# Optimization experiments

Hardware: AMD Instinct MI355X
Metric: run time of the kernel (lower is better)

## Reference

```python
import jax, jax.numpy as jnp
import numpy as np

N, D = 8192, 512
LOGIT_SCALE = 2.659


def setup_inputs() -> dict:
    key = jax.random.key(0)
    k1, k2, k3 = jax.random.split(key, 3)
    text_features = jax.random.normal(k1, (N, D), dtype=jnp.float32)
    image_features = jax.random.normal(k2, (N, D), dtype=jnp.float32)
    labels = jax.random.randint(k3, (N,), 0, 100, dtype=jnp.int64)
    # sprinkle in some -1 (unlabeled) entries like the original supports
    labels = jnp.where(jax.random.uniform(jax.random.fold_in(key, 7), (N,)) < 0.1, -1, labels)
    return {"text_features": text_features, "image_features": image_features, "labels": labels}


def _l2_normalize(x):
    n = jnp.sqrt(jnp.sum(x * x, axis=-1, keepdims=True))
    return x / jnp.maximum(n, 1e-12)


def _soft_ce(s, t):
    # -(t * log softmax(s)).sum(-1) / t.sum(-1), averaged over rows
    loss = -jnp.sum(t * jax.nn.log_softmax(s, axis=-1), axis=-1)
    return jnp.mean(loss / jnp.sum(t, axis=-1))


def reference(text_features, image_features, labels):
    img = _l2_normalize(image_features)
    txt = _l2_normalize(text_features)
    logits_per_image = LOGIT_SCALE * (img @ txt.T)   # [N, N]
    logits_per_text = LOGIT_SCALE * (txt @ img.T)    # [N, N]

    # Vectorized equivalent of the per-row loop:
    # T[i,j] = 1 if i == j else (labels[i] == labels[j] and labels[i] != -1)
    eq = (labels[:, None] == labels[None, :]) & (labels[:, None] != -1)
    n = labels.shape[0]
    target = jnp.where(jnp.eye(n, dtype=bool), 1.0, eq.astype(jnp.float32))

    return (_soft_ce(logits_per_image, target) + _soft_ce(logits_per_text, target)) / 2
```

## Files before the change

kernel.cpp:

```cpp
#include <hip/hip_runtime.h>
#include <hip/hip_bf16.h>

#define N_ROWS 8192
#define DIM 512
#define SCALE 2.659f
#define MAXLOGIT 2.659f
#define LOG2E 1.4426950408889634f
#define NCHUNK 16
#define CHUNK 512
#define BM 128
#define BN 128
#define NCLS 128

typedef __attribute__((ext_vector_type(8))) short short8;
typedef __attribute__((ext_vector_type(4))) float f32x4;

__device__ __forceinline__ unsigned short f2bf(float f) {
    unsigned int u = __float_as_uint(f);
    u += 0x7fffu + ((u >> 16) & 1u);
    return (unsigned short)(u >> 16);
}
__device__ __forceinline__ float bf2f(unsigned short s) {
    return __uint_as_float((unsigned)s << 16);
}

__global__ __launch_bounds__(256) void norm_cast_kernel(
    const float* __restrict__ text, const float* __restrict__ image,
    const int* __restrict__ labels,
    unsigned short* __restrict__ imgn, unsigned short* __restrict__ txtn,
    float4* __restrict__ zbase, float* __restrict__ sd, float* __restrict__ out)
{
    if (blockIdx.x < 16) {
        zbase[blockIdx.x * 256 + threadIdx.x] = make_float4(0.f, 0.f, 0.f, 0.f);
        if (blockIdx.x == 0 && threadIdx.x == 0) out[0] = 0.f;
    }
    int row  = blockIdx.x * 4 + (threadIdx.x >> 6);
    int lane = threadIdx.x & 63;
    const float4* si = (const float4*)(image + (size_t)row * DIM) + lane * 2;
    const float4* st = (const float4*)(text  + (size_t)row * DIM) + lane * 2;
    float4 a = si[0], b = si[1], c = st[0], d = st[1];
    float ssa = a.x*a.x + a.y*a.y + a.z*a.z + a.w*a.w
              + b.x*b.x + b.y*b.y + b.z*b.z + b.w*b.w;
    float sst = c.x*c.x + c.y*c.y + c.z*c.z + c.w*c.w
              + d.x*d.x + d.y*d.y + d.z*d.z + d.w*d.w;
    float sab = a.x*c.x + a.y*c.y + a.z*c.z + a.w*c.w
              + b.x*d.x + b.y*d.y + b.z*d.z + b.w*d.w;
    #pragma unroll
    for (int m = 1; m < 64; m <<= 1) {
        ssa += __shfl_xor(ssa, m, 64);
        sst += __shfl_xor(sst, m, 64);
        sab += __shfl_xor(sab, m, 64);
    }
    float sca = 1.0f / fmaxf(sqrtf(ssa), 1e-12f);
    float sct = 1.0f / fmaxf(sqrtf(sst), 1e-12f);
    uint4 oi, ot;
    oi.x = (unsigned)f2bf(a.x*sca) | ((unsigned)f2bf(a.y*sca) << 16);
    oi.y = (unsigned)f2bf(a.z*sca) | ((unsigned)f2bf(a.w*sca) << 16);
    oi.z = (unsigned)f2bf(b.x*sca) | ((unsigned)f2bf(b.y*sca) << 16);
    oi.w = (unsigned)f2bf(b.z*sca) | ((unsigned)f2bf(b.w*sca) << 16);
    ot.x = (unsigned)f2bf(c.x*sct) | ((unsigned)f2bf(c.y*sct) << 16);
    ot.y = (unsigned)f2bf(c.z*sct) | ((unsigned)f2bf(c.w*sct) << 16);
    ot.z = (unsigned)f2bf(d.x*sct) | ((unsigned)f2bf(d.y*sct) << 16);
    ot.w = (unsigned)f2bf(d.z*sct) | ((unsigned)f2bf(d.w*sct) << 16);
    *((uint4*)(imgn + (size_t)row * DIM) + lane) = oi;
    *((uint4*)(txtn + (size_t)row * DIM) + lane) = ot;
    if (lane == 0)
        sd[row] = (labels[row] < 0) ? sab * sca * sct : 0.0f;
}

__global__ __launch_bounds__(256) void class_sum_kernel(
    const unsigned short* __restrict__ imgn, const unsigned short* __restrict__ txtn,
    const int* __restrict__ labels,
    float* __restrict__ c_txt, float* __restrict__ c_img, int* __restrict__ cnt)
{
    __shared__ int list[512];
    __shared__ int lcount;
    int cls = blockIdx.x & (NCLS - 1);
    int mat = blockIdx.x >> 7;
    const unsigned* src = (const unsigned*)(mat ? imgn : txtn);
    float* dst = mat ? c_img : c_txt;
    int tid = threadIdx.x;
    if (tid == 0) lcount = 0;
    __syncthreads();
    #pragma unroll
    for (int base = 0; base < N_ROWS; base += 256) {
        int lb = labels[base + tid];
        if (lb == cls) { int s = atomicAdd(&lcount, 1); list[s & 511] = base + tid; }
    }
    __syncthreads();
    int m = lcount;
    float a0 = 0.f, a1 = 0.f;
    int r = 0;
    for (; r + 4 <= m; r += 4) {
        unsigned u0 = src[(size_t)list[r]   * (DIM/2) + tid];
        unsigned u1 = src[(size_t)list[r+1] * (DIM/2) + tid];
        unsigned u2 = src[(size_t)list[r+2] * (DIM/2) + tid];
        unsigned u3 = src[(size_t)list[r+3] * (DIM/2) + tid];
        a0 += __uint_as_float((u0 & 0xffffu) << 16) + __uint_as_float((u1 & 0xffffu) << 16)
            + __uint_as_float((u2 & 0xffffu) << 16) + __uint_as_float((u3 & 0xffffu) << 16);
        a1 += __uint_as_float(u0 & 0xffff0000u) + __uint_as_float(u1 & 0xffff0000u)
            + __uint_as_float(u2 & 0xffff0000u) + __uint_as_float(u3 & 0xffff0000u);
    }
    for (; r < m; ++r) {
        unsigned u = src[(size_t)list[r] * (DIM/2) + tid];
        a0 += __uint_as_float((u & 0xffffu) << 16);
        a1 += __uint_as_float(u & 0xffff0000u);
    }
    dst[(size_t)cls * DIM + tid*2]     = a0;
    dst[(size_t)cls * DIM + tid*2 + 1] = a1;
    if (mat == 0 && tid == 0) cnt[cls] = m;
}

#define ASYNC16(gp, lp) \
  __builtin_amdgcn_global_load_lds((const __attribute__((address_space(1))) void*)(gp), \
                                   (__attribute__((address_space(3))) void*)(lp), 16, 0, 0)

#define SFENCE __builtin_amdgcn_sched_barrier(0)

#define STAGE(b, tcol, k0)                                                    \
  {                                                                           \
    const unsigned short* Ap = A + (size_t)(rowBase + w*16 + srow) * DIM      \
                                 + (k0) + spart;                              \
    const unsigned short* Bp = B + (size_t)((tcol) + w*16 + srow) * DIM       \
                                 + (k0) + spart;                              \
    ASYNC16(Ap,            &Ald[b][(w*16) * 32]);                             \
    ASYNC16(Ap + 64 * DIM, &Ald[b][(64 + w*16) * 32]);                        \
    ASYNC16(Bp,            &Bld[b][(w*16) * 32]);                             \
    ASYNC16(Bp + 64 * DIM, &Bld[b][(64 + w*16) * 32]);                        \
  }

#define STEP_SYNC                                                             \
  SFENCE;                                                                     \
  asm volatile("s_waitcnt vmcnt(0)" ::: "memory");                            \
  SFENCE;                                                                     \
  __builtin_amdgcn_s_barrier();                                               \
  SFENCE;

__global__ __launch_bounds__(256, 2) void gemm_fused_kernel(
    const unsigned short* __restrict__ imgn, const unsigned short* __restrict__ txtn,
    float* __restrict__ rs, float* __restrict__ cs)
{
    __shared__ unsigned short Ald[2][BM * 32];
    __shared__ unsigned short Bld[2][BN * 32];
    __shared__ float red[2][BM];
    __shared__ float colb[2][CHUNK];

    int bid    = blockIdx.x;
    int rowblk = bid & 63;
    int chunk  = bid >> 6;
    const unsigned short* A = imgn;
    const unsigned short* B = txtn;
    int rowBase  = rowblk * BM;
    int colBase0 = chunk * CHUNK;

    int tid  = threadIdx.x;
    int lane = tid & 63;
    int w    = tid >> 6;
    int wr   = w >> 1, wc = w & 1;
    int q    = lane >> 4;
    int lm   = lane & 15;

    float s_acc[16];
    #pragma unroll
    for (int i = 0; i < 16; ++i) s_acc[i] = 0.f;

    int srow  = lane >> 2;
    int spart = (lane & 3) * 8;

    const float C1 = SCALE * LOG2E;
    const float C2 = -MAXLOGIT * LOG2E;

    STAGE(0, colBase0, 0);
    STEP_SYNC;

    #pragma unroll 1
    for (int tile = 0; tile < CHUNK / BN; ++tile) {
        int colBase = colBase0 + tile * BN;
        f32x4 acc[4][4];
        #pragma unroll
        for (int mi = 0; mi < 4; ++mi)
          #pragma unroll
          for (int ni = 0; ni < 4; ++ni)
            acc[mi][ni] = (f32x4){0.f, 0.f, 0.f, 0.f};

        #pragma unroll
        for (int kt = 0; kt < DIM / 32; ++kt) {
            const int b = kt & 1;
            if (kt < DIM / 32 - 1) {
                STAGE(b ^ 1, colBase, (kt + 1) * 32);
            } else if (tile < CHUNK / BN - 1) {
                STAGE(b ^ 1, colBase + BN, 0);
            }

            short8 af[4], bf[4];
            #pragma unroll
            for (int mi = 0; mi < 4; ++mi)
                af[mi] = *(const short8*)(&Ald[b][(wr*64 + mi*16 + lm)*32 + q*8]);
            #pragma unroll
            for (int ni = 0; ni < 4; ++ni)
                bf[ni] = *(const short8*)(&Bld[b][(wc*64 + ni*16 + lm)*32 + q*8]);
            #pragma unroll
            for (int mi = 0; mi < 4; ++mi)
              #pragma unroll
              for (int ni = 0; ni < 4; ++ni)
                acc[mi][ni] = __builtin_amdgcn_mfma_f32_16x16x32_bf16(
                                  af[mi], bf[ni], acc[mi][ni], 0, 0, 0);

            if (kt == DIM / 32 - 1) {
                #pragma unroll
                for (int ni = 0; ni < 4; ++ni) {
                    float csum = 0.f;
                    #pragma unroll
                    for (int mi = 0; mi < 4; ++mi) {
                      #pragma unroll
                      for (int r = 0; r < 4; ++r) {
                        float e = __builtin_amdgcn_exp2f(fmaf(acc[mi][ni][r], C1, C2));
                        s_acc[mi*4 + r] += e;
                        csum += e;
                      }
                    }
                    csum += __shfl_xor(csum, 16, 64);
                    csum += __shfl_xor(csum, 32, 64);
                    if (q == 0)
                        colb[wr][tile*BN + wc*64 + ni*16 + lm] = csum;
                }
            }
            STEP_SYNC;
        }
    }

    #pragma unroll
    for (int idx = 0; idx < 16; ++idx) {
        float s = s_acc[idx];
        #pragma unroll
        for (int m = 1; m < 16; m <<= 1) s += __shfl_xor(s, m, 64);
        s_acc[idx] = s;
    }
    if (lm == 0) {
        #pragma unroll
        for (int idx = 0; idx < 16; ++idx) {
            int rl = wr*64 + (idx>>2)*16 + q*4 + (idx&3);
            red[wc][rl] = s_acc[idx];
        }
    }
    __syncthreads();
    if (tid < BM)
        unsafeAtomicAdd(&rs[rowBase + tid], red[0][tid] + red[1][tid]);
    for (int c = tid; c < CHUNK; c += 256)
        unsafeAtomicAdd(&cs[colBase0 + c], colb[0][c] + colb[1][c]);
}

__global__ __launch_bounds__(256) void loss_tail_kernel(
    const float* __restrict__ rs, const float* __restrict__ cs,
    const float* __restrict__ sd, const float* __restrict__ c_txt,
    const float* __restrict__ c_img, const int* __restrict__ cnt,
    float* __restrict__ out)
{
    __shared__ float wsum[4];
    int tid = threadIdx.x, lane = tid & 63, w = tid >> 6;
    int gidx = blockIdx.x * 256 + tid;
    float local;
    if (gidx < N_ROWS)
        local = (MAXLOGIT + logf(rs[gidx])) - 2.0f * SCALE * sd[gidx];
    else
        local = MAXLOGIT + logf(cs[gidx - N_ROWS]);

    int cls = blockIdx.x * 2 + (tid >> 7);
    int e0  = (tid & 127) * 4;
    int n   = cnt[cls];
    if (n > 0) {
        float4 x = *(const float4*)(c_txt + (size_t)cls * DIM + e0);
        float4 y = *(const float4*)(c_img + (size_t)cls * DIM + e0);
        float dotp = x.x*y.x + x.y*y.y + x.z*y.z + x.w*y.w;
        local -= 2.0f * SCALE * dotp / (float)n;
    }

    #pragma unroll
    for (int m = 1; m < 64; m <<= 1) local += __shfl_xor(local, m, 64);
    if (lane == 0) wsum[w] = local;
    __syncthreads();
    if (tid == 0)
        unsafeAtomicAdd(out, (wsum[0] + wsum[1] + wsum[2] + wsum[3])
                             * (1.0f / (2 * N_ROWS)));
}

extern "C" void kernel_launch(void* const* d_in, const int* in_sizes, int n_in,
                              void* d_out, int out_size, void* d_ws, size_t ws_size,
                              hipStream_t stream)
{
    const float* text   = (const float*)d_in[0];
    const float* image  = (const float*)d_in[1];
    const int*   labels = (const int*)d_in[2];

    unsigned short* imgn = (unsigned short*)d_ws;
    unsigned short* txtn = imgn + (size_t)N_ROWS * DIM;
    char* p = (char*)d_ws + 2 * (size_t)N_ROWS * DIM * sizeof(unsigned short);
    float* rs    = (float*)p;
    float* cs    = rs + N_ROWS;
    float* sd    = cs + N_ROWS;
    float* c_txt = sd + N_ROWS;
    float* c_img = c_txt + (size_t)NCLS * DIM;
    int*   cnt   = (int*)(c_img + (size_t)NCLS * DIM);
    float* out = (float*)d_out;

    hipLaunchKernelGGL(norm_cast_kernel, dim3(N_ROWS / 4), dim3(256), 0, stream,
                       text, image, labels, imgn, txtn, (float4*)rs, sd, out);
    hipLaunchKernelGGL(gemm_fused_kernel, dim3(64 * NCHUNK), dim3(256), 0, stream,
                       imgn, txtn, rs, cs);
    hipLaunchKernelGGL(class_sum_kernel, dim3(2 * NCLS), dim3(256), 0, stream,
                       imgn, txtn, labels, c_txt, c_img, cnt);
    hipLaunchKernelGGL(loss_tail_kernel, dim3(64), dim3(256), 0, stream,
                       rs, cs, sd, c_txt, c_img, cnt, out);
}
```

Measured before the change: 193.9 us.

## Triple-buffer GEMM loads and split class sums across row slices with atomics

The GEMM's LDS staging moves from double to triple buffering with prefetch distance two, using partial vmcnt waits so that loads overlap more compute. The launch bound becomes 3 blocks per CU. The class-sum kernel is split across 8 row slices per class and matrix, for 16x more blocks, and accumulates through atomics. This requires zeroing the class buffers, so the workspace layout is reordered and the zeroing in norm_cast is extended. Costs are higher LDS and register pressure in the GEMM and extra atomic traffic in the class sums.

```diff
diff --git a/kernel.cpp b/kernel.cpp
--- a/kernel.cpp
+++ b/kernel.cpp
@@ -15,13 +15,12 @@
 typedef __attribute__((ext_vector_type(8))) short short8;
 typedef __attribute__((ext_vector_type(4))) float f32x4;
 
+#define ZERO_F4 36896
+
 __device__ __forceinline__ unsigned short f2bf(float f) {
     unsigned int u = __float_as_uint(f);
     u += 0x7fffu + ((u >> 16) & 1u);
     return (unsigned short)(u >> 16);
-}
-__device__ __forceinline__ float bf2f(unsigned short s) {
-    return __uint_as_float((unsigned)s << 16);
 }
 
 __global__ __launch_bounds__(256) void norm_cast_kernel(
@@ -30,10 +29,10 @@
     unsigned short* __restrict__ imgn, unsigned short* __restrict__ txtn,
     float4* __restrict__ zbase, float* __restrict__ sd, float* __restrict__ out)
 {
-    if (blockIdx.x < 16) {
-        zbase[blockIdx.x * 256 + threadIdx.x] = make_float4(0.f, 0.f, 0.f, 0.f);
-        if (blockIdx.x == 0 && threadIdx.x == 0) out[0] = 0.f;
-    }
+    int zi = blockIdx.x * 256 + threadIdx.x;
+    if (zi < ZERO_F4) zbase[zi] = make_float4(0.f, 0.f, 0.f, 0.f);
+    if (zi == 0) out[0] = 0.f;
+
     int row  = blockIdx.x * 4 + (threadIdx.x >> 6);
     int lane = threadIdx.x & 63;
     const float4* si = (const float4*)(image + (size_t)row * DIM) + lane * 2;
@@ -73,22 +72,28 @@
     const int* __restrict__ labels,
     float* __restrict__ c_txt, float* __restrict__ c_img, int* __restrict__ cnt)
 {
-    __shared__ int list[512];
+    __shared__ int list[1024];
     __shared__ int lcount;
-    int cls = blockIdx.x & (NCLS - 1);
-    int mat = blockIdx.x >> 7;
+    int blk = blockIdx.x;
+    int cls = blk & (NCLS - 1);
+    int mat = (blk >> 7) & 1;
+    int slc = blk >> 8;
     const unsigned* src = (const unsigned*)(mat ? imgn : txtn);
     float* dst = mat ? c_img : c_txt;
     int tid = threadIdx.x;
     if (tid == 0) lcount = 0;
     __syncthreads();
-    #pragma unroll
-    for (int base = 0; base < N_ROWS; base += 256) {
-        int lb = labels[base + tid];
-        if (lb == cls) { int s = atomicAdd(&lcount, 1); list[s & 511] = base + tid; }
+    int base0 = slc * 1024;
+    #pragma unroll
+    for (int it = 0; it < 4; ++it) {
+        int i  = base0 + it * 256 + tid;
+        int lb = labels[i];
+        if (lb == cls) { int s = atomicAdd(&lcount, 1); list[s] = i; }
     }
     __syncthreads();
     int m = lcount;
+    if (m == 0) return;
+    if (mat == 0 && tid == 0) atomicAdd(&cnt[cls], m);
     float a0 = 0.f, a1 = 0.f;
     int r = 0;
     for (; r + 4 <= m; r += 4) {
@@ -106,9 +111,8 @@
         a0 += __uint_as_float((u & 0xffffu) << 16);
         a1 += __uint_as_float(u & 0xffff0000u);
     }
-    dst[(size_t)cls * DIM + tid*2]     = a0;
-    dst[(size_t)cls * DIM + tid*2 + 1] = a1;
-    if (mat == 0 && tid == 0) cnt[cls] = m;
+    unsafeAtomicAdd(&dst[(size_t)cls * DIM + tid*2],     a0);
+    unsafeAtomicAdd(&dst[(size_t)cls * DIM + tid*2 + 1], a1);
 }
 
 #define ASYNC16(gp, lp) \
@@ -129,19 +133,12 @@
     ASYNC16(Bp + 64 * DIM, &Bld[b][(64 + w*16) * 32]);                        \
   }
 
-#define STEP_SYNC                                                             \
-  SFENCE;                                                                     \
-  asm volatile("s_waitcnt vmcnt(0)" ::: "memory");                            \
-  SFENCE;                                                                     \
-  __builtin_amdgcn_s_barrier();                                               \
-  SFENCE;
-
-__global__ __launch_bounds__(256, 2) void gemm_fused_kernel(
+__global__ __launch_bounds__(256, 3) void gemm_fused_kernel(
     const unsigned short* __restrict__ imgn, const unsigned short* __restrict__ txtn,
     float* __restrict__ rs, float* __restrict__ cs)
 {
-    __shared__ unsigned short Ald[2][BM * 32];
-    __shared__ unsigned short Bld[2][BN * 32];
+    __shared__ unsigned short Ald[3][BM * 32];
+    __shared__ unsigned short Bld[3][BN * 32];
     __shared__ float red[2][BM];
     __shared__ float colb[2][CHUNK];
 
@@ -171,11 +168,17 @@
     const float C2 = -MAXLOGIT * LOG2E;
 
     STAGE(0, colBase0, 0);
-    STEP_SYNC;
+    STAGE(1, colBase0, 32);
+    SFENCE;
+    asm volatile("s_waitcnt vmcnt(4)" ::: "memory");
+    SFENCE;
+    __builtin_amdgcn_s_barrier();
+    SFENCE;
+
+    int bcur = 0;
 
     #pragma unroll 1
     for (int tile = 0; tile < CHUNK / BN; ++tile) {
-        int colBase = colBase0 + tile * BN;
         f32x4 acc[4][4];
         #pragma unroll
         for (int mi = 0; mi < 4; ++mi)
@@ -185,20 +188,20 @@
 
         #pragma unroll
         for (int kt = 0; kt < DIM / 32; ++kt) {
-            const int b = kt & 1;
-            if (kt < DIM / 32 - 1) {
-                STAGE(b ^ 1, colBase, (kt + 1) * 32);
-            } else if (tile < CHUNK / BN - 1) {
-                STAGE(b ^ 1, colBase + BN, 0);
+            int g2 = tile * 16 + kt + 2;
+            if (g2 < 64) {
+                int t2 = g2 >> 4, k2 = g2 & 15;
+                int bpf = bcur + 2; if (bpf >= 3) bpf -= 3;
+                STAGE(bpf, colBase0 + t2 * BN, k2 * 32);
             }
 
             short8 af[4], bf[4];
             #pragma unroll
             for (int mi = 0; mi < 4; ++mi)
-                af[mi] = *(const short8*)(&Ald[b][(wr*64 + mi*16 + lm)*32 + q*8]);
+                af[mi] = *(const short8*)(&Ald[bcur][(wr*64 + mi*16 + lm)*32 + q*8]);
             #pragma unroll
             for (int ni = 0; ni < 4; ++ni)
-                bf[ni] = *(const short8*)(&Bld[b][(wc*64 + ni*16 + lm)*32 + q*8]);
+                bf[ni] = *(const short8*)(&Bld[bcur][(wc*64 + ni*16 + lm)*32 + q*8]);
             #pragma unroll
             for (int mi = 0; mi < 4; ++mi)
               #pragma unroll
@@ -225,7 +228,14 @@
                         colb[wr][tile*BN + wc*64 + ni*16 + lm] = csum;
                 }
             }
-            STEP_SYNC;
+
+            SFENCE;
+            if (g2 < 64) asm volatile("s_waitcnt vmcnt(4)" ::: "memory");
+            else         asm volatile("s_waitcnt vmcnt(0)" ::: "memory");
+            SFENCE;
+            __builtin_amdgcn_s_barrier();
+            SFENCE;
+            bcur = (bcur == 2) ? 0 : bcur + 1;
         }
     }
 
@@ -297,17 +307,17 @@
     char* p = (char*)d_ws + 2 * (size_t)N_ROWS * DIM * sizeof(unsigned short);
     float* rs    = (float*)p;
     float* cs    = rs + N_ROWS;
-    float* sd    = cs + N_ROWS;
-    float* c_txt = sd + N_ROWS;
+    float* c_txt = cs + N_ROWS;
     float* c_img = c_txt + (size_t)NCLS * DIM;
     int*   cnt   = (int*)(c_img + (size_t)NCLS * DIM);
+    float* sd    = (float*)(cnt + NCLS);
     float* out = (float*)d_out;
 
     hipLaunchKernelGGL(norm_cast_kernel, dim3(N_ROWS / 4), dim3(256), 0, stream,
                        text, image, labels, imgn, txtn, (float4*)rs, sd, out);
     hipLaunchKernelGGL(gemm_fused_kernel, dim3(64 * NCHUNK), dim3(256), 0, stream,
                        imgn, txtn, rs, cs);
-    hipLaunchKernelGGL(class_sum_kernel, dim3(2 * NCLS), dim3(256), 0, stream,
+    hipLaunchKernelGGL(class_sum_kernel, dim3(16 * NCLS), dim3(256), 0, stream,
                        imgn, txtn, labels, c_txt, c_img, cnt);
     hipLaunchKernelGGL(loss_tail_kernel, dim3(64), dim3(256), 0, stream,
                        rs, cs, sd, c_txt, c_img, cnt, out);
```

Measured after the change: 223.4 us. 1.15x slower.
